# Performance work log

Hardware: AMD Instinct MI355X
Metric: run time of the kernel (lower is better)

The kernel has to match this reference:

```python
import jax, jax.numpy as jnp
import numpy as np

B, M, P, OUT_DIM, DIM = 4096, 128, 3, 256, 3  # batch, n_ctrl_pts, degree, eval points, coord dim
KNOTS = M + P + 1  # clamped knot vector length = 132


def setup_inputs() -> dict:
    key = jax.random.key(0)
    k1, k2 = jax.random.split(key)
    ctrl_pts = jax.random.normal(k1, (B, M, DIM), dtype=jnp.float32)
    # Clamped, nondecreasing knot vector in [0,1]: (p+1) zeros, sorted interior, (p+1) ones.
    interior = jnp.sort(jax.random.uniform(k2, (B, M - P - 1), dtype=jnp.float32), axis=1)
    knot_u = jnp.concatenate(
        [jnp.zeros((B, P + 1), jnp.float32), interior, jnp.ones((B, P + 1), jnp.float32)],
        axis=1,
    )
    return {"ctrl_pts": ctrl_pts, "knot_u": knot_u}


def reference(ctrl_pts, knot_u):
    p = P
    U = knot_u  # [B, m+p+1]
    u = jnp.linspace(1e-05, 1.0 - 1e-05, OUT_DIM, dtype=jnp.float32)  # [T] shared across batch

    # --- knot-span search (argmin of masked positive differences, first occurrence) ---
    d = u[None, None, :] - U[:, p:, None]            # [B, m+1, T]
    masked = jnp.where(d > 1e-08, d, 1.0)
    uspan = jnp.argmin(masked, axis=1) + p           # [B, T], int

    # --- Cox-de Boor basis recursion (degree 0 .. p) ---
    Ni = [None] * (p + 1)
    Ni[0] = jnp.ones((U.shape[0], OUT_DIM), jnp.float32)
    for k in range(1, p + 1):
        saved = jnp.zeros((U.shape[0], OUT_DIM), jnp.float32)
        for r in range(k):
            U1 = jnp.take_along_axis(U, uspan + r + 1, axis=1)      # U[s, uspan + r + 1]
            U2 = jnp.take_along_axis(U, uspan + 1 - k + r, axis=1)  # U[s, uspan + 1 - k + r]
            dU = (U1 - u) + (u - U2)
            dU_ = jnp.where(dU == 0.0, 1e-04, dU)
            temp = Ni[r] / dU_
            temp = jnp.where(dU == 0.0, 1e-04, temp)
            Ni[r] = saved + (U1 - u) * temp
            saved = (u - U2) * temp
        Ni[k] = saved
    Nu = jnp.stack(Ni, axis=-1)  # [B, T, p+1] nonzero basis values

    # --- sparse combine: instead of scattering into a [B,T,m] matrix and a dense matmul,
    # gather the (p+1) active control points per eval point (same math: all other
    # basis entries are zero) ---
    idx = uspan[:, :, None] + jnp.arange(-p, 1)                     # [B, T, p+1]
    cp = ctrl_pts[jnp.arange(U.shape[0])[:, None, None], idx]      # [B, T, p+1, DIM]
    return jnp.einsum('btk,btkd->btd', Nu, cp.astype(jnp.float32))  # [B, T, DIM]
```

## Files before the change

### kernel.cpp

```cpp
#include <hip/hip_runtime.h>


#define B_N     4096
#define M_N     128
#define P_DEG   3
#define T_N     256
#define KNOTS_N 132

__global__ __launch_bounds__(256) void curve_eval_kernel(
    const float* __restrict__ ctrl,
    const float* __restrict__ knots,
    float* __restrict__ out)
{
    __shared__ float Uk[KNOTS_N];
    __shared__ float cp[M_N * 4];

    const int b = blockIdx.x;
    const int t = threadIdx.x;

    if (t < 33) {
        ((float4*)Uk)[t] = ((const float4*)(knots + (size_t)b * KNOTS_N))[t];
    }
    if (t < 96) {
        float4 v = ((const float4*)(ctrl + (size_t)b * (M_N * 3)))[t];
        int i = t * 4;
        cp[((i + 0) / 3) * 4 + (i + 0) % 3] = v.x;
        cp[((i + 1) / 3) * 4 + (i + 1) % 3] = v.y;
        cp[((i + 2) / 3) * 4 + (i + 2) % 3] = v.z;
        cp[((i + 3) / 3) * 4 + (i + 3) % 3] = v.w;
    }
    __syncthreads();

    const double start = 1e-5;
    const double stop  = 1.0 - 1e-5;
    const double step  = (stop - start) / 255.0;
    float u;
    if (t == T_N - 1) u = (float)stop;
    else              u = (float)((double)t * step + start);

    int lo = 0, hi = 128;
    while (lo < hi) {
        int mid = (lo + hi + 1) >> 1;
        float d = __fsub_rn(u, Uk[P_DEG + mid]);
        if (d > 1e-8f) lo = mid; else hi = mid - 1;
    }
    {
        const float dmin = __fsub_rn(u, Uk[P_DEG + lo]);
        while (lo > 0 && __fsub_rn(u, Uk[P_DEG + lo - 1]) == dmin) --lo;
    }
    const int span = lo + P_DEG;

    const float w0 = Uk[span - 2];
    const float w1 = Uk[span - 1];
    const float w2 = Uk[span];
    const float w3 = Uk[span + 1];
    const float w4 = Uk[span + 2];
    const float w5 = Uk[span + 3];

    const float A1 = __fsub_rn(w3, u);
    const float A2 = __fsub_rn(w4, u);
    const float A3 = __fsub_rn(w5, u);
    const float B0 = __fsub_rn(u, w0);
    const float B1 = __fsub_rn(u, w1);
    const float B2 = __fsub_rn(u, w2);

    #define TDIV(N_, a1_, a2_, OUT_)                                    \
        {                                                               \
            const float dU = __fadd_rn(a1_, a2_);                       \
            float tmp = __fmul_rn((N_), __builtin_amdgcn_rcpf(dU));     \
            if (dU == 0.0f) tmp = 1e-4f;                                \
            OUT_ = tmp;                                                 \
        }

    float t0, t1, t2;
    float N0, N1, N2, N3, saved;

    TDIV(1.0f, A1, B2, t0);
    N0 = __fmul_rn(A1, t0);
    N1 = __fmul_rn(B2, t0);
    TDIV(N0, A1, B1, t0);
    TDIV(N1, A2, B2, t1);
    N0    = __fmul_rn(A1, t0);
    saved = __fmul_rn(B1, t0);
    N1    = __fadd_rn(saved, __fmul_rn(A2, t1));
    N2    = __fmul_rn(B2, t1);
    TDIV(N0, A1, B0, t0);
    TDIV(N1, A2, B1, t1);
    TDIV(N2, A3, B2, t2);
    N0    = __fmul_rn(A1, t0);
    saved = __fmul_rn(B0, t0);
    N1    = __fadd_rn(saved, __fmul_rn(A2, t1));
    saved = __fmul_rn(B1, t1);
    N2    = __fadd_rn(saved, __fmul_rn(A3, t2));
    N3    = __fmul_rn(B2, t2);
    #undef TDIV

    const float4 c0 = *(const float4*)&cp[(span - 3) * 4];
    const float4 c1 = *(const float4*)&cp[(span - 2) * 4];
    const float4 c2 = *(const float4*)&cp[(span - 1) * 4];
    const float4 c3 = *(const float4*)&cp[(span - 0) * 4];

    float acc0, acc1, acc2;
    acc0 = __fmul_rn(N0, c0.x);
    acc1 = __fmul_rn(N0, c0.y);
    acc2 = __fmul_rn(N0, c0.z);
    acc0 = __fadd_rn(acc0, __fmul_rn(N1, c1.x));
    acc1 = __fadd_rn(acc1, __fmul_rn(N1, c1.y));
    acc2 = __fadd_rn(acc2, __fmul_rn(N1, c1.z));
    acc0 = __fadd_rn(acc0, __fmul_rn(N2, c2.x));
    acc1 = __fadd_rn(acc1, __fmul_rn(N2, c2.y));
    acc2 = __fadd_rn(acc2, __fmul_rn(N2, c2.z));
    acc0 = __fadd_rn(acc0, __fmul_rn(N3, c3.x));
    acc1 = __fadd_rn(acc1, __fmul_rn(N3, c3.y));
    acc2 = __fadd_rn(acc2, __fmul_rn(N3, c3.z));

    float* o = out + ((size_t)b * T_N + t) * 3;
    o[0] = acc0;
    o[1] = acc1;
    o[2] = acc2;
}

extern "C" void kernel_launch(void* const* d_in, const int* in_sizes, int n_in,
                              void* d_out, int out_size, void* d_ws, size_t ws_size,
                              hipStream_t stream) {
    const float* ctrl  = (const float*)d_in[0];
    const float* knots = (const float*)d_in[1];
    float* out = (float*)d_out;

    curve_eval_kernel<<<dim3(B_N), dim3(T_N), 0, stream>>>(ctrl, knots, out);
}
```

Baseline: 11.93 us.

## Process four curves per block with interleaved branchless binary searches

Each block now handles four batch curves instead of one, loading their knots and control points into shared memory together and launching a quarter as many blocks. The knot-span binary search becomes a fixed-step, unrolled search run for all four curves side by side, which exposes independent LDS loads and removes data-dependent loop control. This amortises block launch and sync overhead and raises instruction-level parallelism, at the cost of more registers and shared memory per block and fewer blocks overall to spread across CUs.

Result: slower. 12.46 us (+4.4%).

```diff
diff --git a/kernel.cpp b/kernel.cpp
--- a/kernel.cpp
+++ b/kernel.cpp
@@ -6,28 +6,32 @@
 #define P_DEG   3
 #define T_N     256
 #define KNOTS_N 132
+#define CPB     4
 
-__global__ __launch_bounds__(256) void curve_eval_kernel(
+__global__ __launch_bounds__(256, 4) void curve_eval_kernel(
     const float* __restrict__ ctrl,
     const float* __restrict__ knots,
     float* __restrict__ out)
 {
-    __shared__ float Uk[KNOTS_N];
-    __shared__ float cp[M_N * 4];
+    __shared__ float Uk[CPB][KNOTS_N];
+    __shared__ float cp[CPB][M_N * 4];
 
-    const int b = blockIdx.x;
-    const int t = threadIdx.x;
+    const int b0 = blockIdx.x * CPB;
+    const int t  = threadIdx.x;
 
-    if (t < 33) {
-        ((float4*)Uk)[t] = ((const float4*)(knots + (size_t)b * KNOTS_N))[t];
+    if (t < CPB * 33) {
+        const int c = t / 33, j = t - c * 33;
+        ((float4*)Uk[c])[j] =
+            ((const float4*)(knots + (size_t)(b0 + c) * KNOTS_N))[j];
     }
-    if (t < 96) {
-        float4 v = ((const float4*)(ctrl + (size_t)b * (M_N * 3)))[t];
-        int i = t * 4;
-        cp[((i + 0) / 3) * 4 + (i + 0) % 3] = v.x;
-        cp[((i + 1) / 3) * 4 + (i + 1) % 3] = v.y;
-        cp[((i + 2) / 3) * 4 + (i + 2) % 3] = v.z;
-        cp[((i + 3) / 3) * 4 + (i + 3) % 3] = v.w;
+    for (int i = t; i < CPB * 96; i += 256) {
+        const int c = i / 96, j = i - c * 96;
+        float4 v = ((const float4*)(ctrl + (size_t)(b0 + c) * (M_N * 3)))[j];
+        const int e = j * 4;
+        cp[c][((e + 0) / 3) * 4 + (e + 0) % 3] = v.x;
+        cp[c][((e + 1) / 3) * 4 + (e + 1) % 3] = v.y;
+        cp[c][((e + 2) / 3) * 4 + (e + 2) % 3] = v.z;
+        cp[c][((e + 3) / 3) * 4 + (e + 3) % 3] = v.w;
     }
     __syncthreads();
 
@@ -38,86 +42,98 @@
     if (t == T_N - 1) u = (float)stop;
     else              u = (float)((double)t * step + start);
 
-    int lo = 0, hi = 128;
-    while (lo < hi) {
-        int mid = (lo + hi + 1) >> 1;
-        float d = __fsub_rn(u, Uk[P_DEG + mid]);
-        if (d > 1e-8f) lo = mid; else hi = mid - 1;
+    int lo[CPB];
+    #pragma unroll
+    for (int c = 0; c < CPB; ++c) lo[c] = 0;
+    #pragma unroll
+    for (int s = 128; s >= 1; s >>= 1) {
+        #pragma unroll
+        for (int c = 0; c < CPB; ++c) {
+            const int cand = lo[c] + s;
+            const int idx  = cand <= 128 ? cand : 128;
+            const float d  = __fsub_rn(u, Uk[c][P_DEG + idx]);
+            if (cand <= 128 && d > 1e-8f) lo[c] = cand;
+        }
     }
-    {
-        const float dmin = __fsub_rn(u, Uk[P_DEG + lo]);
-        while (lo > 0 && __fsub_rn(u, Uk[P_DEG + lo - 1]) == dmin) --lo;
+    #pragma unroll
+    for (int c = 0; c < CPB; ++c) {
+        const float dmin = __fsub_rn(u, Uk[c][P_DEG + lo[c]]);
+        while (lo[c] > 0 && __fsub_rn(u, Uk[c][P_DEG + lo[c] - 1]) == dmin)
+            --lo[c];
     }
-    const int span = lo + P_DEG;
 
-    const float w0 = Uk[span - 2];
-    const float w1 = Uk[span - 1];
-    const float w2 = Uk[span];
-    const float w3 = Uk[span + 1];
-    const float w4 = Uk[span + 2];
-    const float w5 = Uk[span + 3];
+    #pragma unroll
+    for (int c = 0; c < CPB; ++c) {
+        const int span = lo[c] + P_DEG;
 
-    const float A1 = __fsub_rn(w3, u);
-    const float A2 = __fsub_rn(w4, u);
-    const float A3 = __fsub_rn(w5, u);
-    const float B0 = __fsub_rn(u, w0);
-    const float B1 = __fsub_rn(u, w1);
-    const float B2 = __fsub_rn(u, w2);
+        const float w0 = Uk[c][span - 2];
+        const float w1 = Uk[c][span - 1];
+        const float w2 = Uk[c][span];
+        const float w3 = Uk[c][span + 1];
+        const float w4 = Uk[c][span + 2];
+        const float w5 = Uk[c][span + 3];
 
-    #define TDIV(N_, a1_, a2_, OUT_)                                    \
-        {                                                               \
-            const float dU = __fadd_rn(a1_, a2_);                       \
-            float tmp = __fmul_rn((N_), __builtin_amdgcn_rcpf(dU));     \
-            if (dU == 0.0f) tmp = 1e-4f;                                \
-            OUT_ = tmp;                                                 \
-        }
+        const float A1 = __fsub_rn(w3, u);
+        const float A2 = __fsub_rn(w4, u);
+        const float A3 = __fsub_rn(w5, u);
+        const float B0 = __fsub_rn(u, w0);
+        const float B1 = __fsub_rn(u, w1);
+        const float B2 = __fsub_rn(u, w2);
 
-    float t0, t1, t2;
-    float N0, N1, N2, N3, saved;
+        #define TDIV(N_, a1_, a2_, OUT_)                                \
+            {                                                           \
+                const float dU = __fadd_rn(a1_, a2_);                   \
+                float tmp = __fmul_rn((N_), __builtin_amdgcn_rcpf(dU)); \
+                if (dU == 0.0f) tmp = 1e-4f;                            \
+                OUT_ = tmp;                                             \
+            }
 
-    TDIV(1.0f, A1, B2, t0);
-    N0 = __fmul_rn(A1, t0);
-    N1 = __fmul_rn(B2, t0);
-    TDIV(N0, A1, B1, t0);
-    TDIV(N1, A2, B2, t1);
-    N0    = __fmul_rn(A1, t0);
-    saved = __fmul_rn(B1, t0);
-    N1    = __fadd_rn(saved, __fmul_rn(A2, t1));
-    N2    = __fmul_rn(B2, t1);
-    TDIV(N0, A1, B0, t0);
-    TDIV(N1, A2, B1, t1);
-    TDIV(N2, A3, B2, t2);
-    N0    = __fmul_rn(A1, t0);
-    saved = __fmul_rn(B0, t0);
-    N1    = __fadd_rn(saved, __fmul_rn(A2, t1));
-    saved = __fmul_rn(B1, t1);
-    N2    = __fadd_rn(saved, __fmul_rn(A3, t2));
-    N3    = __fmul_rn(B2, t2);
-    #undef TDIV
+        float t0, t1, t2;
+        float N0, N1, N2, N3, saved;
+        TDIV(1.0f, A1, B2, t0);
+        N0 = __fmul_rn(A1, t0);
+        N1 = __fmul_rn(B2, t0);
+        TDIV(N0, A1, B1, t0);
+        TDIV(N1, A2, B2, t1);
+        N0    = __fmul_rn(A1, t0);
+        saved = __fmul_rn(B1, t0);
+        N1    = __fadd_rn(saved, __fmul_rn(A2, t1));
+        N2    = __fmul_rn(B2, t1);
+        TDIV(N0, A1, B0, t0);
+        TDIV(N1, A2, B1, t1);
+        TDIV(N2, A3, B2, t2);
+        N0    = __fmul_rn(A1, t0);
+        saved = __fmul_rn(B0, t0);
+        N1    = __fadd_rn(saved, __fmul_rn(A2, t1));
+        saved = __fmul_rn(B1, t1);
+        N2    = __fadd_rn(saved, __fmul_rn(A3, t2));
+        N3    = __fmul_rn(B2, t2);
+        #undef TDIV
 
-    const float4 c0 = *(const float4*)&cp[(span - 3) * 4];
-    const float4 c1 = *(const float4*)&cp[(span - 2) * 4];
-    const float4 c2 = *(const float4*)&cp[(span - 1) * 4];
-    const float4 c3 = *(const float4*)&cp[(span - 0) * 4];
+        const float4 c0 = *(const float4*)&cp[c][(span - 3) * 4];
+        const float4 c1 = *(const float4*)&cp[c][(span - 2) * 4];
+        const float4 c2 = *(const float4*)&cp[c][(span - 1) * 4];
+        const float4 c3 = *(const float4*)&cp[c][(span - 0) * 4];
 
-    float acc0, acc1, acc2;
-    acc0 = __fmul_rn(N0, c0.x);
-    acc1 = __fmul_rn(N0, c0.y);
-    acc2 = __fmul_rn(N0, c0.z);
-    acc0 = __fadd_rn(acc0, __fmul_rn(N1, c1.x));
-    acc1 = __fadd_rn(acc1, __fmul_rn(N1, c1.y));
-    acc2 = __fadd_rn(acc2, __fmul_rn(N1, c1.z));
-    acc0 = __fadd_rn(acc0, __fmul_rn(N2, c2.x));
-    acc1 = __fadd_rn(acc1, __fmul_rn(N2, c2.y));
-    acc2 = __fadd_rn(acc2, __fmul_rn(N2, c2.z));
-    acc0 = __fadd_rn(acc0, __fmul_rn(N3, c3.x));
-    acc1 = __fadd_rn(acc1, __fmul_rn(N3, c3.y));
-    acc2 = __fadd_rn(acc2, __fmul_rn(N3, c3.z));
+        float acc0, acc1, acc2;
+        acc0 = __fmul_rn(N0, c0.x);
+        acc1 = __fmul_rn(N0, c0.y);
+        acc2 = __fmul_rn(N0, c0.z);
+        acc0 = __fadd_rn(acc0, __fmul_rn(N1, c1.x));
+        acc1 = __fadd_rn(acc1, __fmul_rn(N1, c1.y));
+        acc2 = __fadd_rn(acc2, __fmul_rn(N1, c1.z));
+        acc0 = __fadd_rn(acc0, __fmul_rn(N2, c2.x));
+        acc1 = __fadd_rn(acc1, __fmul_rn(N2, c2.y));
+        acc2 = __fadd_rn(acc2, __fmul_rn(N2, c2.z));
+        acc0 = __fadd_rn(acc0, __fmul_rn(N3, c3.x));
+        acc1 = __fadd_rn(acc1, __fmul_rn(N3, c3.y));
+        acc2 = __fadd_rn(acc2, __fmul_rn(N3, c3.z));
 
-    float* o = out + ((size_t)b * T_N + t) * 3;
-    o[0] = acc0;
-    o[1] = acc1;
-    o[2] = acc2;
+        float* o = out + ((size_t)(b0 + c) * T_N + t) * 3;
+        o[0] = acc0;
+        o[1] = acc1;
+        o[2] = acc2;
+    }
 }
 
 extern "C" void kernel_launch(void* const* d_in, const int* in_sizes, int n_in,
@@ -127,5 +143,5 @@
     const float* knots = (const float*)d_in[1];
     float* out = (float*)d_out;
 
-    curve_eval_kernel<<<dim3(B_N), dim3(T_N), 0, stream>>>(ctrl, knots, out);
+    curve_eval_kernel<<<dim3(B_N / CPB), dim3(T_N), 0, stream>>>(ctrl, knots, out);
 }
```
